# Kernel optimization log

Measured on AMD Instinct MI355X. Metric: run time of the kernel, lower is better.

## Reference

```python
import jax, jax.numpy as jnp
import numpy as np

N_HEADS = 16
EMB_DIM = 1024
HEAD_DIM = EMB_DIM // N_HEADS


def setup_inputs() -> dict:
    key = jax.random.key(0)
    k1, k2, k3, k4, k5 = jax.random.split(key, 5)
    s = 1.0 / np.sqrt(EMB_DIM)
    return {
        "attn_in": jax.random.normal(k1, (4, 2048, EMB_DIM), dtype=jnp.float32),
        "W_qkv": jax.random.uniform(k2, (EMB_DIM, 3 * EMB_DIM), jnp.float32, -s, s),
        "b_qkv": jax.random.uniform(k3, (3 * EMB_DIM,), jnp.float32, -s, s),
        "W_out": jax.random.uniform(k4, (EMB_DIM, EMB_DIM), jnp.float32, -s, s),
        "b_out": jax.random.uniform(k5, (EMB_DIM,), jnp.float32, -s, s),
    }


def reference(attn_in, W_qkv, b_qkv, W_out, b_out):
    N, L, E = attn_in.shape
    qkv = attn_in @ W_qkv + b_qkv                      # [N, L, 3E]
    q, k, v = jnp.split(qkv, 3, axis=-1)
    # [N, L, E] -> [N, H, L, D]
    def heads(x):
        return x.reshape(N, L, N_HEADS, HEAD_DIM).transpose(0, 2, 1, 3)
    q, k, v = heads(q), heads(k), heads(v)
    scale = 1.0 / np.sqrt(HEAD_DIM)
    scores = jnp.einsum('nhqd,nhkd->nhqk', q, k) * scale   # [N, H, L, L]
    attn = jax.nn.softmax(scores, axis=-1)
    o = jnp.einsum('nhqk,nhkd->nhqd', attn, v)             # [N, H, L, D]
    o = o.transpose(0, 2, 1, 3).reshape(N, L, E)
    return o @ W_out + b_out
```

## Files before the change

### kernel.cpp

```cpp
#include <hip/hip_runtime.h>

typedef __attribute__((ext_vector_type(8))) short short8;
typedef __attribute__((ext_vector_type(4))) float f32x4;
typedef __attribute__((ext_vector_type(16))) float f32x16;

#define MFMA16(A,B,C) __builtin_amdgcn_mfma_f32_16x16x32_bf16(A,B,C,0,0,0)
#define MFMA32(A,B,C) __builtin_amdgcn_mfma_f32_32x32x16_bf16(A,B,C,0,0,0)

__device__ __forceinline__ short f2bf(float f){
  union { float f; unsigned int u; } v; v.f = f;
  unsigned int u = v.u;
  unsigned int r = (u + 0x7fffu + ((u >> 16) & 1u)) >> 16;
  return (short)r;
}

typedef const __attribute__((address_space(1))) void* gptr_t;
typedef __attribute__((address_space(3))) void* lptr_t;

__device__ __forceinline__ void gload16(const short* g, short* l){
  __builtin_amdgcn_global_load_lds((gptr_t)g, (lptr_t)l, 16, 0, 0);
}


__global__ __launch_bounds__(256) void cvt_x_kernel(const float* __restrict__ x,
                                                    short* __restrict__ xb){
  const size_t i = (size_t)blockIdx.x * 256 + threadIdx.x;
  const float4* p = (const float4*)x + i * 2;
  float4 a = p[0], b = p[1];
  short8 o;
  o[0]=f2bf(a.x); o[1]=f2bf(a.y); o[2]=f2bf(a.z); o[3]=f2bf(a.w);
  o[4]=f2bf(b.x); o[5]=f2bf(b.y); o[6]=f2bf(b.z); o[7]=f2bf(b.w);
  *(short8*)(xb + i * 8) = o;
}

__global__ __launch_bounds__(256) void cvt_t_kernel(const float* __restrict__ src,
                                                    short* __restrict__ dst,
                                                    int R, int C){
  __shared__ float tile[32][33];
  const int tx = threadIdx.x, ty = threadIdx.y;
  const int c0 = blockIdx.x * 32, r0 = blockIdx.y * 32;
  #pragma unroll
  for (int i = 0; i < 32; i += 8)
    tile[ty + i][tx] = src[(size_t)(r0 + ty + i) * C + c0 + tx];
  __syncthreads();
  #pragma unroll
  for (int i = 0; i < 32; i += 8)
    dst[(size_t)(c0 + ty + i) * R + r0 + tx] = f2bf(tile[tx][ty + i]);
}


template<int EPI>
__global__ __launch_bounds__(256) void gemm_bt(
    const short* __restrict__ A, const short* __restrict__ BT,
    const float* __restrict__ bias,
    float* __restrict__ Cf,
    short* __restrict__ q_ws, short* __restrict__ k_ws, short* __restrict__ vt_ws)
{
  __shared__ __align__(16) short As[4096];
  __shared__ __align__(16) short Bs[4096];
  const int tid = threadIdx.x;
  const int bm = blockIdx.x, bn = blockIdx.y;
  const int lane = tid & 63, wid = tid >> 6;
  const int wr = wid >> 1, wc = wid & 1;
  const int r = lane & 15, g = lane >> 4;

  f32x4 acc[4][4] = {};

  const short* ag = A  + (size_t)(bm * 128 + (tid >> 2)) * 1024 + (tid & 3) * 8;
  const short* bg = BT + (size_t)(bn * 128 + (tid >> 2)) * 1024 + (tid & 3) * 8;
  short* asd = &As[tid * 8];
  short* bsd = &Bs[tid * 8];

  for (int kk = 0; kk < 32; ++kk){
    gload16(ag + kk * 32,             asd);
    gload16(ag + kk * 32 + 64 * 1024, asd + 2048);
    gload16(bg + kk * 32,             bsd);
    gload16(bg + kk * 32 + 64 * 1024, bsd + 2048);
    asm volatile("s_waitcnt vmcnt(0)" ::: "memory");
    __syncthreads();
    short8 a[4], b[4];
    #pragma unroll
    for (int mf = 0; mf < 4; ++mf)
      a[mf] = *(const short8*)&As[(wr * 64 + mf * 16 + r) * 32 + g * 8];
    #pragma unroll
    for (int nf = 0; nf < 4; ++nf)
      b[nf] = *(const short8*)&Bs[(wc * 64 + nf * 16 + r) * 32 + g * 8];
    #pragma unroll
    for (int mf = 0; mf < 4; ++mf)
      #pragma unroll
      for (int nf = 0; nf < 4; ++nf)
        acc[mf][nf] = MFMA16(a[mf], b[nf], acc[mf][nf]);
    __syncthreads();
  }

  if (EPI == 0){
    #pragma unroll
    for (int nf = 0; nf < 4; ++nf){
      const int c = bn * 128 + wc * 64 + nf * 16 + r;
      const float bv = bias[c];
      const int type = c >> 10;
      const int h = (c & 1023) >> 6, d = c & 63;
      const float mul = (type == 0) ? 0.18033688011112042f : 1.0f;
      #pragma unroll
      for (int mf = 0; mf < 4; ++mf){
        const int row0 = bm * 128 + wr * 64 + mf * 16 + g * 4;
        const int nb = row0 >> 11, l0 = row0 & 2047;
        f32x4 v = acc[mf][nf];
        if (type == 2){
          short4 pk;
          pk.x = f2bf(v[0] + bv); pk.y = f2bf(v[1] + bv);
          pk.z = f2bf(v[2] + bv); pk.w = f2bf(v[3] + bv);
          *(short4*)&vt_ws[((size_t)(nb * 16 + h) * 64 + d) * 2048 + l0] = pk;
        } else {
          short* dst = (type == 0) ? q_ws : k_ws;
          const size_t base = ((size_t)(nb * 16 + h) * 2048 + l0) * 64 + d;
          #pragma unroll
          for (int j = 0; j < 4; ++j)
            dst[base + (size_t)j * 64] = f2bf((v[j] + bv) * mul);
        }
      }
    }
  } else {
    #pragma unroll
    for (int nf = 0; nf < 4; ++nf){
      const int c = bn * 128 + wc * 64 + nf * 16 + r;
      const float bv = bias[c];
      #pragma unroll
      for (int mf = 0; mf < 4; ++mf){
        const int row0 = bm * 128 + wr * 64 + mf * 16 + g * 4;
        f32x4 v = acc[mf][nf];
        #pragma unroll
        for (int j = 0; j < 4; ++j)
          Cf[(size_t)(row0 + j) * 1024 + c] = v[j] + bv;
      }
    }
  }
}


__global__ __launch_bounds__(512, 4) void attn_kernel(
    const short* __restrict__ qw, const short* __restrict__ kw,
    const short* __restrict__ vtw, short* __restrict__ ow)
{
  __shared__ __align__(16) short Ks[4][4096];
  __shared__ __align__(16) short Vs[4][4096];

  const int id = blockIdx.x;
  const int xcd = id & 7, j2 = id >> 3;
  const int nh = xcd * 8 + (j2 & 7);
  const int qt = j2 >> 3;
  const int tid = threadIdx.x;
  const int lane = tid & 63, w = tid >> 6;
  const int l31 = lane & 31, hi = lane >> 5, w7 = lane & 7;

  const size_t hoff = (size_t)nh * 2048 * 64;
  const short* kh = kw + hoff;
  const short* vh = vtw + hoff;

  const int srow = tid >> 3, schunk = tid & 7;
  const int scw = (schunk ^ (srow & 7)) * 8;
  const short* ksrc = kh + srow * 64 + scw;
  const short* vsrc = vh + (size_t)srow * 2048 + scw;

  unsigned aoffh[2][4];
  #pragma unroll
  for (int T = 0; T < 2; ++T)
    #pragma unroll
    for (int s = 0; s < 4; ++s)
      aoffh[T][s] = (unsigned)((l31 + 32 * T) * 64 + (((2 * s + hi) ^ w7) * 8));

  const int qrow0 = qt * 256 + w * 32;
  short8 qfr[4];
  #pragma unroll
  for (int s = 0; s < 4; ++s)
    qfr[s] = *(const short8*)(qw + hoff + (size_t)(qrow0 + l31) * 64 + s * 16 + hi * 8);

  f32x16 oa0 = {}, oa1 = {}, lacc = {};
  short8 onesB;
  #pragma unroll
  for (int i = 0; i < 8; ++i) onesB[i] = (short)0x3F80;

  gload16(ksrc,        &Ks[0][tid * 8]);
  gload16(vsrc,        &Vs[0][tid * 8]);
  gload16(ksrc + 4096, &Ks[1][tid * 8]);
  gload16(vsrc + 64,   &Vs[1][tid * 8]);
  gload16(ksrc + 8192, &Ks[2][tid * 8]);
  gload16(vsrc + 128,  &Vs[2][tid * 8]);

  for (int t4 = 0; t4 < 32; t4 += 4){
    #pragma unroll
    for (int u = 0; u < 4; ++u){
      const int t = t4 + u;
      asm volatile("s_waitcnt vmcnt(4)" ::: "memory");
      __builtin_amdgcn_s_barrier();
      {
        const int ts = (t + 3) & 31;
        gload16(ksrc + ts * 4096, &Ks[(u + 3) & 3][tid * 8]);
        gload16(vsrc + ts * 64,   &Vs[(u + 3) & 3][tid * 8]);
      }
      const short* Kb = &Ks[u][0];
      const short* Vb = &Vs[u][0];

      f32x16 ss0, ss1;
      {
        short8 k0 = *(const short8*)&Kb[aoffh[0][0]];
        short8 k1 = *(const short8*)&Kb[aoffh[1][0]];
        const f32x16 zz = {};
        ss0 = MFMA32(k0, qfr[0], zz);
        ss1 = MFMA32(k1, qfr[0], zz);
      }
      #pragma unroll
      for (int s = 1; s < 4; ++s){
        short8 k0 = *(const short8*)&Kb[aoffh[0][s]];
        short8 k1 = *(const short8*)&Kb[aoffh[1][s]];
        ss0 = MFMA32(k0, qfr[s], ss0);
        ss1 = MFMA32(k1, qfr[s], ss1);
      }

      unsigned u0[8], u1[8];
      #pragma unroll
      for (int m = 0; m < 8; ++m){
        float a = exp2f(ss0[2 * m]), b = exp2f(ss0[2 * m + 1]);
        asm("v_cvt_pk_bf16_f32 %0, %1, %2" : "=v"(u0[m]) : "v"(a), "v"(b));
        float c = exp2f(ss1[2 * m]), d = exp2f(ss1[2 * m + 1]);
        asm("v_cvt_pk_bf16_f32 %0, %1, %2" : "=v"(u1[m]) : "v"(c), "v"(d));
      }

      short8 pa[4];
      #pragma unroll
      for (int s = 0; s < 4; ++s){
        const int sg = (s & 1) * 4;
        unsigned a0 = (s < 2) ? u0[sg + 0] : u1[sg + 0];
        unsigned a1 = (s < 2) ? u0[sg + 1] : u1[sg + 1];
        unsigned a2 = (s < 2) ? u0[sg + 2] : u1[sg + 2];
        unsigned a3 = (s < 2) ? u0[sg + 3] : u1[sg + 3];
        asm("v_permlane32_swap_b32 %0, %1" : "+v"(a0), "+v"(a2));
        asm("v_permlane32_swap_b32 %0, %1" : "+v"(a1), "+v"(a3));
        union { unsigned q[4]; short8 s8; } cv;
        cv.q[0] = a0; cv.q[1] = a1; cv.q[2] = a2; cv.q[3] = a3;
        pa[s] = cv.s8;
      }

      #pragma unroll
      for (int s = 0; s < 4; ++s){
        short8 v0 = *(const short8*)&Vb[aoffh[0][s]];
        short8 v1 = *(const short8*)&Vb[aoffh[1][s]];
        oa0 = MFMA32(pa[s], v0, oa0);
        oa1 = MFMA32(pa[s], v1, oa1);
        lacc = MFMA32(pa[s], onesB, lacc);
      }
    }
  }

  const int n = nh >> 4, h = nh & 15;
  #pragma unroll
  for (int j = 0; j < 16; ++j){
    const float inv = 1.0f / lacc[j];
    const int qr = (j & 3) + 8 * (j >> 2) + 4 * hi;
    const size_t base = ((size_t)n * 2048 + qrow0 + qr) * 1024 + h * 64 + l31;
    ow[base]      = f2bf(oa0[j] * inv);
    ow[base + 32] = f2bf(oa1[j] * inv);
  }
}


extern "C" void kernel_launch(void* const* d_in, const int* in_sizes, int n_in,
                              void* d_out, int out_size, void* d_ws, size_t ws_size,
                              hipStream_t stream){
  const float* attn_in = (const float*)d_in[0];
  const float* W_qkv   = (const float*)d_in[1];
  const float* b_qkv   = (const float*)d_in[2];
  const float* W_out   = (const float*)d_in[3];
  const float* b_out   = (const float*)d_in[4];
  float* out = (float*)d_out;

  char* ws = (char*)d_ws;
  short* xb    = (short*)(ws);
  short* wqT   = (short*)(ws + 16777216);
  short* woT   = (short*)(ws + 23068672);
  short* q_ws  = (short*)(ws + 25165824);
  short* k_ws  = (short*)(ws + 41943040);
  short* vt_ws = (short*)(ws + 58720256);
  short* o_ws  = (short*)(ws + 75497472);

  cvt_x_kernel<<<4096, 256, 0, stream>>>(attn_in, xb);
  cvt_t_kernel<<<dim3(96, 32), dim3(32, 8), 0, stream>>>(W_qkv, wqT, 1024, 3072);
  cvt_t_kernel<<<dim3(32, 32), dim3(32, 8), 0, stream>>>(W_out, woT, 1024, 1024);
  gemm_bt<0><<<dim3(64, 24), 256, 0, stream>>>(xb, wqT, b_qkv, nullptr, q_ws, k_ws, vt_ws);
  attn_kernel<<<512, 512, 0, stream>>>(q_ws, k_ws, vt_ws, o_ws);
  gemm_bt<1><<<dim3(64, 8), 256, 0, stream>>>(o_ws, woT, b_out, out, nullptr, nullptr, nullptr);
}
```

Baseline: 208.3 us.

## Drop LDS staging in attention, read K/V tiles directly from global memory

The attention kernel no longer stages K and V through a 4-deep LDS ring with global_load_lds and barriers. Each wave now reads its MFMA fragments straight from global memory, relying on L1/L2 caching. V^T is stored tile-blocked (64x64 per key tile) so each key tile is contiguous. Blocks shrink to 4 waves covering 128 query rows, doubling the grid. This removes barrier and LDS traffic but gives up the software prefetch pipeline and cross-wave reuse in LDS, so the loop may stall on global load latency.

```diff
diff --git a/kernel.cpp b/kernel.cpp
--- a/kernel.cpp
+++ b/kernel.cpp
@@ -110,7 +110,8 @@
           short4 pk;
           pk.x = f2bf(v[0] + bv); pk.y = f2bf(v[1] + bv);
           pk.z = f2bf(v[2] + bv); pk.w = f2bf(v[3] + bv);
-          *(short4*)&vt_ws[((size_t)(nb * 16 + h) * 64 + d) * 2048 + l0] = pk;
+          const int head = nb * 16 + h;
+          *(short4*)&vt_ws[(((size_t)head * 32 + (l0 >> 6)) * 64 + d) * 64 + (l0 & 63)] = pk;
         } else {
           short* dst = (type == 0) ? q_ws : k_ws;
           const size_t base = ((size_t)(nb * 16 + h) * 2048 + l0) * 64 + d;
@@ -138,38 +139,30 @@
 }
 
 
-__global__ __launch_bounds__(512, 4) void attn_kernel(
+__global__ __launch_bounds__(256) void attn_kernel(
     const short* __restrict__ qw, const short* __restrict__ kw,
     const short* __restrict__ vtw, short* __restrict__ ow)
 {
-  __shared__ __align__(16) short Ks[4][4096];
-  __shared__ __align__(16) short Vs[4][4096];
-
   const int id = blockIdx.x;
-  const int xcd = id & 7, j2 = id >> 3;
-  const int nh = xcd * 8 + (j2 & 7);
-  const int qt = j2 >> 3;
+  const int xcd = id & 7;
+  const int nh = xcd * 8 + ((id >> 3) & 7);
+  const int qt = id >> 6;
   const int tid = threadIdx.x;
   const int lane = tid & 63, w = tid >> 6;
-  const int l31 = lane & 31, hi = lane >> 5, w7 = lane & 7;
+  const int l31 = lane & 31, hi = lane >> 5;
 
   const size_t hoff = (size_t)nh * 2048 * 64;
   const short* kh = kw + hoff;
   const short* vh = vtw + hoff;
 
-  const int srow = tid >> 3, schunk = tid & 7;
-  const int scw = (schunk ^ (srow & 7)) * 8;
-  const short* ksrc = kh + srow * 64 + scw;
-  const short* vsrc = vh + (size_t)srow * 2048 + scw;
-
-  unsigned aoffh[2][4];
+  unsigned off[2][4];
   #pragma unroll
   for (int T = 0; T < 2; ++T)
     #pragma unroll
     for (int s = 0; s < 4; ++s)
-      aoffh[T][s] = (unsigned)((l31 + 32 * T) * 64 + (((2 * s + hi) ^ w7) * 8));
-
-  const int qrow0 = qt * 256 + w * 32;
+      off[T][s] = (unsigned)((l31 + 32 * T) * 64 + 16 * s + 8 * hi);
+
+  const int qrow0 = qt * 128 + w * 32;
   short8 qfr[4];
   #pragma unroll
   for (int s = 0; s < 4; ++s)
@@ -180,75 +173,57 @@
   #pragma unroll
   for (int i = 0; i < 8; ++i) onesB[i] = (short)0x3F80;
 
-  gload16(ksrc,        &Ks[0][tid * 8]);
-  gload16(vsrc,        &Vs[0][tid * 8]);
-  gload16(ksrc + 4096, &Ks[1][tid * 8]);
-  gload16(vsrc + 64,   &Vs[1][tid * 8]);
-  gload16(ksrc + 8192, &Ks[2][tid * 8]);
-  gload16(vsrc + 128,  &Vs[2][tid * 8]);
-
-  for (int t4 = 0; t4 < 32; t4 += 4){
-    #pragma unroll
-    for (int u = 0; u < 4; ++u){
-      const int t = t4 + u;
-      asm volatile("s_waitcnt vmcnt(4)" ::: "memory");
-      __builtin_amdgcn_s_barrier();
-      {
-        const int ts = (t + 3) & 31;
-        gload16(ksrc + ts * 4096, &Ks[(u + 3) & 3][tid * 8]);
-        gload16(vsrc + ts * 64,   &Vs[(u + 3) & 3][tid * 8]);
-      }
-      const short* Kb = &Ks[u][0];
-      const short* Vb = &Vs[u][0];
-
-      f32x16 ss0, ss1;
-      {
-        short8 k0 = *(const short8*)&Kb[aoffh[0][0]];
-        short8 k1 = *(const short8*)&Kb[aoffh[1][0]];
-        const f32x16 zz = {};
-        ss0 = MFMA32(k0, qfr[0], zz);
-        ss1 = MFMA32(k1, qfr[0], zz);
-      }
-      #pragma unroll
-      for (int s = 1; s < 4; ++s){
-        short8 k0 = *(const short8*)&Kb[aoffh[0][s]];
-        short8 k1 = *(const short8*)&Kb[aoffh[1][s]];
-        ss0 = MFMA32(k0, qfr[s], ss0);
-        ss1 = MFMA32(k1, qfr[s], ss1);
-      }
-
-      unsigned u0[8], u1[8];
-      #pragma unroll
-      for (int m = 0; m < 8; ++m){
-        float a = exp2f(ss0[2 * m]), b = exp2f(ss0[2 * m + 1]);
-        asm("v_cvt_pk_bf16_f32 %0, %1, %2" : "=v"(u0[m]) : "v"(a), "v"(b));
-        float c = exp2f(ss1[2 * m]), d = exp2f(ss1[2 * m + 1]);
-        asm("v_cvt_pk_bf16_f32 %0, %1, %2" : "=v"(u1[m]) : "v"(c), "v"(d));
-      }
-
-      short8 pa[4];
-      #pragma unroll
-      for (int s = 0; s < 4; ++s){
-        const int sg = (s & 1) * 4;
-        unsigned a0 = (s < 2) ? u0[sg + 0] : u1[sg + 0];
-        unsigned a1 = (s < 2) ? u0[sg + 1] : u1[sg + 1];
-        unsigned a2 = (s < 2) ? u0[sg + 2] : u1[sg + 2];
-        unsigned a3 = (s < 2) ? u0[sg + 3] : u1[sg + 3];
-        asm("v_permlane32_swap_b32 %0, %1" : "+v"(a0), "+v"(a2));
-        asm("v_permlane32_swap_b32 %0, %1" : "+v"(a1), "+v"(a3));
-        union { unsigned q[4]; short8 s8; } cv;
-        cv.q[0] = a0; cv.q[1] = a1; cv.q[2] = a2; cv.q[3] = a3;
-        pa[s] = cv.s8;
-      }
-
-      #pragma unroll
-      for (int s = 0; s < 4; ++s){
-        short8 v0 = *(const short8*)&Vb[aoffh[0][s]];
-        short8 v1 = *(const short8*)&Vb[aoffh[1][s]];
-        oa0 = MFMA32(pa[s], v0, oa0);
-        oa1 = MFMA32(pa[s], v1, oa1);
-        lacc = MFMA32(pa[s], onesB, lacc);
-      }
+  for (int kt = 0; kt < 32; ++kt){
+    const short* kb = kh + kt * 4096;
+    const short* vb = vh + kt * 4096;
+
+    f32x16 ss0, ss1;
+    {
+      short8 k0 = *(const short8*)(kb + off[0][0]);
+      short8 k1 = *(const short8*)(kb + off[1][0]);
+      const f32x16 zz = {};
+      ss0 = MFMA32(k0, qfr[0], zz);
+      ss1 = MFMA32(k1, qfr[0], zz);
+    }
+    #pragma unroll
+    for (int s = 1; s < 4; ++s){
+      short8 k0 = *(const short8*)(kb + off[0][s]);
+      short8 k1 = *(const short8*)(kb + off[1][s]);
+      ss0 = MFMA32(k0, qfr[s], ss0);
+      ss1 = MFMA32(k1, qfr[s], ss1);
+    }
+
+    unsigned u0[8], u1[8];
+    #pragma unroll
+    for (int m = 0; m < 8; ++m){
+      float a = exp2f(ss0[2 * m]), b = exp2f(ss0[2 * m + 1]);
+      asm("v_cvt_pk_bf16_f32 %0, %1, %2" : "=v"(u0[m]) : "v"(a), "v"(b));
+      float c = exp2f(ss1[2 * m]), d = exp2f(ss1[2 * m + 1]);
+      asm("v_cvt_pk_bf16_f32 %0, %1, %2" : "=v"(u1[m]) : "v"(c), "v"(d));
+    }
+
+    short8 pa[4];
+    #pragma unroll
+    for (int s = 0; s < 4; ++s){
+      const int sg = (s & 1) * 4;
+      unsigned a0 = (s < 2) ? u0[sg + 0] : u1[sg + 0];
+      unsigned a1 = (s < 2) ? u0[sg + 1] : u1[sg + 1];
+      unsigned a2 = (s < 2) ? u0[sg + 2] : u1[sg + 2];
+      unsigned a3 = (s < 2) ? u0[sg + 3] : u1[sg + 3];
+      asm("v_permlane32_swap_b32 %0, %1" : "+v"(a0), "+v"(a2));
+      asm("v_permlane32_swap_b32 %0, %1" : "+v"(a1), "+v"(a3));
+      union { unsigned q[4]; short8 s8; } cv;
+      cv.q[0] = a0; cv.q[1] = a1; cv.q[2] = a2; cv.q[3] = a3;
+      pa[s] = cv.s8;
+    }
+
+    #pragma unroll
+    for (int s = 0; s < 4; ++s){
+      short8 v0 = *(const short8*)(vb + off[0][s]);
+      short8 v1 = *(const short8*)(vb + off[1][s]);
+      oa0 = MFMA32(pa[s], v0, oa0);
+      oa1 = MFMA32(pa[s], v1, oa1);
+      lacc = MFMA32(pa[s], onesB, lacc);
     }
   }
 
@@ -287,6 +262,6 @@
   cvt_t_kernel<<<dim3(96, 32), dim3(32, 8), 0, stream>>>(W_qkv, wqT, 1024, 3072);
   cvt_t_kernel<<<dim3(32, 32), dim3(32, 8), 0, stream>>>(W_out, woT, 1024, 1024);
   gemm_bt<0><<<dim3(64, 24), 256, 0, stream>>>(xb, wqT, b_qkv, nullptr, q_ws, k_ws, vt_ws);
-  attn_kernel<<<512, 512, 0, stream>>>(q_ws, k_ws, vt_ws, o_ws);
+  attn_kernel<<<1024, 256, 0, stream>>>(q_ws, k_ws, vt_ws, o_ws);
   gemm_bt<1><<<dim3(64, 8), 256, 0, stream>>>(o_ws, woT, b_out, out, nullptr, nullptr, nullptr);
 }
```

Measured after the change: 346.1 us. +66.2%, slower.

## Tile transposed V workspace into contiguous 64x64 blocks for attention loads

Applied to the files above, without the earlier changes.

The QKV epilogue now writes transposed V into per-tile blocks ([head][tile][d][64 l]), so each 64-key V tile is one contiguous 8KB chunk instead of 64 rows strided by 2048 elements. The attention kernel's V async loads now use the same contiguous addressing as K, which should improve DRAM and cache locality. The change also swaps the inline-asm permlane32_swap for the compiler builtin and uses an asm s_barrier with a memory clobber, which may let the compiler schedule around these instructions differently.

```diff
diff --git a/kernel.cpp b/kernel.cpp
--- a/kernel.cpp
+++ b/kernel.cpp
@@ -110,7 +110,8 @@
           short4 pk;
           pk.x = f2bf(v[0] + bv); pk.y = f2bf(v[1] + bv);
           pk.z = f2bf(v[2] + bv); pk.w = f2bf(v[3] + bv);
-          *(short4*)&vt_ws[((size_t)(nb * 16 + h) * 64 + d) * 2048 + l0] = pk;
+          const int head = nb * 16 + h;
+          *(short4*)&vt_ws[(((size_t)head * 32 + (l0 >> 6)) * 64 + d) * 64 + (l0 & 63)] = pk;
         } else {
           short* dst = (type == 0) ? q_ws : k_ws;
           const size_t base = ((size_t)(nb * 16 + h) * 2048 + l0) * 64 + d;
@@ -160,7 +161,7 @@
   const int srow = tid >> 3, schunk = tid & 7;
   const int scw = (schunk ^ (srow & 7)) * 8;
   const short* ksrc = kh + srow * 64 + scw;
-  const short* vsrc = vh + (size_t)srow * 2048 + scw;
+  const short* vsrc = vh + srow * 64 + scw;
 
   unsigned aoffh[2][4];
   #pragma unroll
@@ -183,38 +184,34 @@
   gload16(ksrc,        &Ks[0][tid * 8]);
   gload16(vsrc,        &Vs[0][tid * 8]);
   gload16(ksrc + 4096, &Ks[1][tid * 8]);
-  gload16(vsrc + 64,   &Vs[1][tid * 8]);
+  gload16(vsrc + 4096, &Vs[1][tid * 8]);
   gload16(ksrc + 8192, &Ks[2][tid * 8]);
-  gload16(vsrc + 128,  &Vs[2][tid * 8]);
+  gload16(vsrc + 8192, &Vs[2][tid * 8]);
 
   for (int t4 = 0; t4 < 32; t4 += 4){
     #pragma unroll
     for (int u = 0; u < 4; ++u){
       const int t = t4 + u;
       asm volatile("s_waitcnt vmcnt(4)" ::: "memory");
-      __builtin_amdgcn_s_barrier();
+      asm volatile("s_barrier" ::: "memory");
       {
         const int ts = (t + 3) & 31;
         gload16(ksrc + ts * 4096, &Ks[(u + 3) & 3][tid * 8]);
-        gload16(vsrc + ts * 64,   &Vs[(u + 3) & 3][tid * 8]);
+        gload16(vsrc + ts * 4096, &Vs[(u + 3) & 3][tid * 8]);
       }
       const short* Kb = &Ks[u][0];
       const short* Vb = &Vs[u][0];
 
       f32x16 ss0, ss1;
       {
-        short8 k0 = *(const short8*)&Kb[aoffh[0][0]];
-        short8 k1 = *(const short8*)&Kb[aoffh[1][0]];
         const f32x16 zz = {};
-        ss0 = MFMA32(k0, qfr[0], zz);
-        ss1 = MFMA32(k1, qfr[0], zz);
+        ss0 = MFMA32(*(const short8*)&Kb[aoffh[0][0]], qfr[0], zz);
+        ss1 = MFMA32(*(const short8*)&Kb[aoffh[1][0]], qfr[0], zz);
       }
       #pragma unroll
       for (int s = 1; s < 4; ++s){
-        short8 k0 = *(const short8*)&Kb[aoffh[0][s]];
-        short8 k1 = *(const short8*)&Kb[aoffh[1][s]];
-        ss0 = MFMA32(k0, qfr[s], ss0);
-        ss1 = MFMA32(k1, qfr[s], ss1);
+        ss0 = MFMA32(*(const short8*)&Kb[aoffh[0][s]], qfr[s], ss0);
+        ss1 = MFMA32(*(const short8*)&Kb[aoffh[1][s]], qfr[s], ss1);
       }
 
       unsigned u0[8], u1[8];
@@ -234,19 +231,18 @@
         unsigned a1 = (s < 2) ? u0[sg + 1] : u1[sg + 1];
         unsigned a2 = (s < 2) ? u0[sg + 2] : u1[sg + 2];
         unsigned a3 = (s < 2) ? u0[sg + 3] : u1[sg + 3];
-        asm("v_permlane32_swap_b32 %0, %1" : "+v"(a0), "+v"(a2));
-        asm("v_permlane32_swap_b32 %0, %1" : "+v"(a1), "+v"(a3));
+        auto r02 = __builtin_amdgcn_permlane32_swap(a0, a2, false, false);
+        auto r13 = __builtin_amdgcn_permlane32_swap(a1, a3, false, false);
         union { unsigned q[4]; short8 s8; } cv;
-        cv.q[0] = a0; cv.q[1] = a1; cv.q[2] = a2; cv.q[3] = a3;
+        cv.q[0] = (unsigned)r02[0]; cv.q[1] = (unsigned)r13[0];
+        cv.q[2] = (unsigned)r02[1]; cv.q[3] = (unsigned)r13[1];
         pa[s] = cv.s8;
       }
 
       #pragma unroll
       for (int s = 0; s < 4; ++s){
-        short8 v0 = *(const short8*)&Vb[aoffh[0][s]];
-        short8 v1 = *(const short8*)&Vb[aoffh[1][s]];
-        oa0 = MFMA32(pa[s], v0, oa0);
-        oa1 = MFMA32(pa[s], v1, oa1);
+        oa0  = MFMA32(pa[s], *(const short8*)&Vb[aoffh[0][s]], oa0);
+        oa1  = MFMA32(pa[s], *(const short8*)&Vb[aoffh[1][s]], oa1);
         lacc = MFMA32(pa[s], onesB, lacc);
       }
     }
```

Measured after the change: 207.6 us. Within noise of the previous version (-0.3%).
